# Performance work log

Hardware: AMD Instinct MI355X
Metric: run time of the kernel (lower is better)

The kernel has to match this reference:

```python
import jax, jax.numpy as jnp
import numpy as np


def setup_inputs() -> dict:
    key = jax.random.key(0)
    k1, k2 = jax.random.split(key)
    N, D, K = 262144, 64, 1024
    residual = jax.random.normal(k1, (N, D), dtype=jnp.float32)
    # nn.init.uniform_(codebook.weight, -1/K, 1/K)
    codebook = jax.random.uniform(k2, (K, D), dtype=jnp.float32,
                                  minval=-1.0 / K, maxval=1.0 / K)
    return {"residual": residual, "codebook": codebook}


def reference(residual, codebook):
    # squared L2 distances via ||a||^2 + ||b||^2 - 2 a.b (argmin-equivalent to
    # the broadcast (N,K,D) form, without materializing it)
    r2 = jnp.sum(residual * residual, axis=1, keepdims=True)        # (N, 1)
    c2 = jnp.sum(codebook * codebook, axis=1)[None, :]              # (1, K)
    dists = r2 + c2 - 2.0 * (residual @ codebook.T)                 # (N, K)
    codes = jnp.argmin(dists, axis=1)                               # (N,) int
    quantized = codebook[codes]                                     # (N, D)
    return quantized, codes
```

## Files before the change

kernel.cpp:

```cpp
#include <hip/hip_runtime.h>
#include <float.h>

#define D 64

typedef float f32x4 __attribute__((ext_vector_type(4)));
typedef _Float16 f16x8 __attribute__((ext_vector_type(8)));

__device__ __forceinline__ float np_sum_sq_64(const float* v) {
  float s[8];
#pragma unroll
  for (int j = 0; j < 8; ++j) s[j] = __fmul_rn(v[j], v[j]);
#pragma unroll
  for (int b = 1; b < 8; ++b) {
#pragma unroll
    for (int j = 0; j < 8; ++j)
      s[j] = __fadd_rn(s[j], __fmul_rn(v[8 * b + j], v[8 * b + j]));
  }
  float t01 = __fadd_rn(s[0], s[1]);
  float t23 = __fadd_rn(s[2], s[3]);
  float t45 = __fadd_rn(s[4], s[5]);
  float t67 = __fadd_rn(s[6], s[7]);
  return __fadd_rn(__fadd_rn(t01, t23), __fadd_rn(t45, t67));
}

__device__ __forceinline__ unsigned int pkh(float a, float b) {
  union { _Float16 h[2]; unsigned int u; } x;
  x.h[0] = (_Float16)a;
  x.h[1] = (_Float16)b;
  return x.u;
}

__global__ __launch_bounds__(64) void vq_prep(
    const float* __restrict__ cb, unsigned short* __restrict__ cbh,
    float4* __restrict__ cbT4, float* __restrict__ c2,
    float* __restrict__ c2n, unsigned int* __restrict__ counters, int K) {
  if (blockIdx.x == 0 && threadIdx.x == 0) { counters[0] = 0u; counters[1] = 0u; }
  int k = blockIdx.x * 64 + threadIdx.x;
  if (k >= K) return;
  float row[D];
  const float4* cp = (const float4*)(cb + (size_t)k * D);
#pragma unroll
  for (int i = 0; i < 16; ++i) {
    float4 v = cp[i];
    row[4 * i] = v.x; row[4 * i + 1] = v.y;
    row[4 * i + 2] = v.z; row[4 * i + 3] = v.w;
    cbT4[(size_t)i * K + k] = v;
    *(uint2*)(cbh + (size_t)k * D + 4 * i) =
        make_uint2(pkh(v.x * 1024.f, v.y * 1024.f),
                   pkh(v.z * 1024.f, v.w * 1024.f));
  }
  float c2v = np_sum_sq_64(row);
  c2[k] = c2v;
  c2n[k] = -512.0f * c2v;
}

__global__ __launch_bounds__(256, 3) void vq_screen(
    const float* __restrict__ residual, const float* __restrict__ codebook,
    const unsigned short* __restrict__ cbh, const float* __restrict__ c2n,
    const float* __restrict__ c2, float* __restrict__ out_q,
    float* __restrict__ codes_f, unsigned int* __restrict__ counters,
    int* __restrict__ list, int N, int K) {
  __shared__ unsigned short smem[4096];
  __shared__ float red[768];
  __shared__ int code_lds[64];
  __shared__ float srow[64];

  int tid = threadIdx.x;
  int rowbase = blockIdx.x * 64;

  float sr4[4];
#pragma unroll
  for (int jj = 0; jj < 4; ++jj) {
    int i = tid + 256 * jj;
    int r = i >> 4, d0 = (i & 15) * 4;
    float4 v = *(const float4*)(residual + (size_t)(rowbase + r) * D + d0);
    sr4[jj] = fabsf(v.x) + fabsf(v.y) + fabsf(v.z) + fabsf(v.w);
    int tile = r >> 4, rr = r & 15;
    int kblk = d0 >> 5, kk = d0 & 31;
    int lanep = rr + 16 * (kk >> 3);
    int off = ((tile * 2 + kblk) * 64 + lanep) * 8 + (kk & 7);
    *(uint2*)(smem + off) = make_uint2(pkh(v.x, v.y), pkh(v.z, v.w));
  }
#pragma unroll
  for (int jj = 0; jj < 4; ++jj) {
    float s = sr4[jj];
    s += __shfl_xor(s, 1, 64);
    s += __shfl_xor(s, 2, 64);
    s += __shfl_xor(s, 4, 64);
    s += __shfl_xor(s, 8, 64);
    sr4[jj] = s;
  }
  if ((tid & 15) == 0) {
#pragma unroll
    for (int jj = 0; jj < 4; ++jj) srow[(tid >> 4) + 16 * jj] = sr4[jj];
  }
  __syncthreads();

  int w = tid >> 6, lane = tid & 63;
  int lane15 = lane & 15, lq = lane >> 4;

  f16x8 ah[4][2];
#pragma unroll
  for (int t = 0; t < 4; ++t)
#pragma unroll
    for (int kb = 0; kb < 2; ++kb)
      ah[t][kb] = *(const f16x8*)(smem + ((t * 2 + kb) * 64 + lane) * 8);

  float m1[4][4], m2[4][4], m3[4][4];
#pragma unroll
  for (int t = 0; t < 4; ++t)
#pragma unroll
    for (int j = 0; j < 4; ++j) {
      m1[t][j] = -FLT_MAX; m2[t][j] = -FLT_MAX; m3[t][j] = -FLT_MAX;
    }

  const unsigned short* ph = cbh + (size_t)(w * 16 + lane15) * D + lq * 8;
  const float* pc2 = c2n + (w * 16 + lane15);

  f16x8 B0a = *(const f16x8*)(ph);
  f16x8 B1a = *(const f16x8*)(ph + 32);
  float c2a = *pc2;
  ph += 64 * D; pc2 += 64;
  f16x8 B0b = *(const f16x8*)(ph);
  f16x8 B1b = *(const f16x8*)(ph + 32);
  float c2b = *pc2;

  unsigned int idb = (unsigned int)((w << 4) | lane15);
  for (int cc = 0; cc < 16; ++cc) {
    f16x8 ch0 = B0a, ch1 = B1a;
    float q = c2a;
    B0a = B0b; B1a = B1b; c2a = c2b;
    if (cc < 14) {
      ph += 64 * D; pc2 += 64;
      B0b = *(const f16x8*)(ph);
      B1b = *(const f16x8*)(ph + 32);
      c2b = *pc2;
    }

#pragma unroll
    for (int t = 0; t < 4; ++t) {
      f32x4 a = {q, q, q, q};
      a = __builtin_amdgcn_mfma_f32_16x16x32_f16(ah[t][0], ch0, a, 0, 0, 0);
      a = __builtin_amdgcn_mfma_f32_16x16x32_f16(ah[t][1], ch1, a, 0, 0, 0);
#pragma unroll
      for (int j = 0; j < 4; ++j) {
        float spf = __uint_as_float((__float_as_uint(a[j]) & 0xFFFFFC00u) | idb);
        float o1 = m1[t][j], o2 = m2[t][j];
        m3[t][j] = __builtin_amdgcn_fmed3f(o2, m3[t][j], spf);
        m2[t][j] = __builtin_amdgcn_fmed3f(o1, o2, spf);
        m1[t][j] = fmaxf(o1, spf);
      }
    }
    idb += 64u;
  }

#pragma unroll
  for (int dlt = 1; dlt < 16; dlt <<= 1) {
#pragma unroll
    for (int t = 0; t < 4; ++t)
#pragma unroll
      for (int j = 0; j < 4; ++j) {
        float a1 = m1[t][j], a2 = m2[t][j], a3 = m3[t][j];
        float b1 = __shfl_xor(a1, dlt, 64);
        float b2 = __shfl_xor(a2, dlt, 64);
        float b3 = __shfl_xor(a3, dlt, 64);
        m1[t][j] = fmaxf(a1, b1);
        m2[t][j] = fmaxf(fminf(a1, b1), fmaxf(a2, b2));
        m3[t][j] = fmaxf(fmaxf(fminf(a2, b1), fminf(a1, b2)), fmaxf(a3, b3));
      }
  }

  if (lane15 == 0) {
#pragma unroll
    for (int t = 0; t < 4; ++t)
#pragma unroll
      for (int j = 0; j < 4; ++j) {
        int r = t * 16 + lq * 4 + j;
        int base = (w * 64 + r) * 3;
        red[base + 0] = m1[t][j];
        red[base + 1] = m2[t][j];
        red[base + 2] = m3[t][j];
      }
  }
  __syncthreads();
  if (tid < 64) {
    float a1 = red[tid * 3 + 0], a2 = red[tid * 3 + 1], a3 = red[tid * 3 + 2];
#pragma unroll
    for (int wv = 1; wv < 4; ++wv) {
      float b1 = red[(wv * 64 + tid) * 3 + 0];
      float b2 = red[(wv * 64 + tid) * 3 + 1];
      float b3 = red[(wv * 64 + tid) * 3 + 2];
      float n1 = fmaxf(a1, b1);
      float n2 = fmaxf(fminf(a1, b1), fmaxf(a2, b2));
      float n3 = fmaxf(fmaxf(fminf(a2, b1), fminf(a1, b2)), fmaxf(a3, b3));
      a1 = n1; a2 = n2; a3 = n3;
    }
    unsigned int u1 = __float_as_uint(a1);
    unsigned int u2 = __float_as_uint(a2);
    unsigned int u3 = __float_as_uint(a3);
    int ka = (int)(u1 & 1023u);
    float g1 = __uint_as_float(u1 & 0xFFFFFC00u);
    float g2 = __uint_as_float(u2 & 0xFFFFFC00u);
    float g3 = __uint_as_float(u3 & 0xFFFFFC00u);
    float margin = __builtin_fmaf(srow[tid], 2.3552e-3f, 2.048e-2f);
    int row = rowbase + tid;
    int win = ka;
    if (g1 - g2 < margin) {
      if (g1 - g3 < margin) {
        unsigned int s = atomicAdd(counters + 0, 1u);
        list[s] = row;
      } else {
        int kb = (int)(u2 & 1023u);
        float r[D];
        const float4* rp = (const float4*)(residual + ((size_t)row << 6));
#pragma unroll
        for (int qq = 0; qq < 16; ++qq) {
          float4 v = rp[qq];
          r[4 * qq] = v.x; r[4 * qq + 1] = v.y;
          r[4 * qq + 2] = v.z; r[4 * qq + 3] = v.w;
        }
        float r2 = np_sum_sq_64(r);
        float da = 0.f, db = 0.f;
        const float4* ap = (const float4*)(codebook + ((size_t)ka << 6));
        const float4* bp = (const float4*)(codebook + ((size_t)kb << 6));
#pragma unroll
        for (int qq = 0; qq < 16; ++qq) {
          float4 x = ap[qq], y = bp[qq];
          da = __fmaf_rn(r[4 * qq + 0], x.x, da); db = __fmaf_rn(r[4 * qq + 0], y.x, db);
          da = __fmaf_rn(r[4 * qq + 1], x.y, da); db = __fmaf_rn(r[4 * qq + 1], y.y, db);
          da = __fmaf_rn(r[4 * qq + 2], x.z, da); db = __fmaf_rn(r[4 * qq + 2], y.z, db);
          da = __fmaf_rn(r[4 * qq + 3], x.w, da); db = __fmaf_rn(r[4 * qq + 3], y.w, db);
        }
        float dista = __fsub_rn(__fadd_rn(r2, c2[ka]), __fmul_rn(2.0f, da));
        float distb = __fsub_rn(__fadd_rn(r2, c2[kb]), __fmul_rn(2.0f, db));
        bool bwin = (distb < dista) || (distb == dista && kb < ka);
        win = bwin ? kb : ka;
      }
    }
    code_lds[tid] = win;
    codes_f[row] = (float)win;
  }
  __syncthreads();

  for (int e = tid; e < 4096; e += 256) {
    int r = e >> 6, d = e & 63;
    out_q[(size_t)rowbase * D + e] = codebook[((size_t)code_lds[r] << 6) + d];
  }
}

__global__ __launch_bounds__(256) void vq_rescore(
    const float* __restrict__ residual, const float* __restrict__ codebook,
    const float4* __restrict__ cbT4, const float* __restrict__ c2,
    float* __restrict__ codes_f, float* __restrict__ out_q,
    const unsigned int* __restrict__ counters,
    const int* __restrict__ list, int K) {
  unsigned int cnt = counters[0];
  int w = threadIdx.x >> 6, lane = threadIdx.x & 63;
  unsigned int npairs = (cnt + 1) >> 1;
  for (unsigned int g = blockIdx.x * 4 + w; g < npairs; g += gridDim.x * 4) {
    int n0 = list[2 * g];
    bool two = (2 * g + 1 < cnt);
    int n1 = two ? list[2 * g + 1] : n0;

    float rl0 = residual[(size_t)n0 * D + lane];
    float rl1 = residual[(size_t)n1 * D + lane];

    int j = lane & 7;
    float x0 = __shfl(rl0, j, 64), x1 = __shfl(rl1, j, 64);
    float s0 = __fmul_rn(x0, x0), s1 = __fmul_rn(x1, x1);
#pragma unroll
    for (int b = 1; b < 8; ++b) {
      x0 = __shfl(rl0, 8 * b + j, 64);
      x1 = __shfl(rl1, 8 * b + j, 64);
      s0 = __fadd_rn(s0, __fmul_rn(x0, x0));
      s1 = __fadd_rn(s1, __fmul_rn(x1, x1));
    }
    s0 = __fadd_rn(s0, __shfl_xor(s0, 1, 64));
    s1 = __fadd_rn(s1, __shfl_xor(s1, 1, 64));
    s0 = __fadd_rn(s0, __shfl_xor(s0, 2, 64));
    s1 = __fadd_rn(s1, __shfl_xor(s1, 2, 64));
    s0 = __fadd_rn(s0, __shfl_xor(s0, 4, 64));
    s1 = __fadd_rn(s1, __shfl_xor(s1, 4, 64));
    float r2_0 = s0, r2_1 = s1;

    float m0[16], m1v[16];
#pragma unroll
    for (int ch = 0; ch < 16; ++ch) { m0[ch] = 0.f; m1v[ch] = 0.f; }

    for (int d4 = 0; d4 < 16; ++d4) {
      float a0 = __shfl(rl0, 4 * d4, 64), b0 = __shfl(rl0, 4 * d4 + 1, 64);
      float c0 = __shfl(rl0, 4 * d4 + 2, 64), e0 = __shfl(rl0, 4 * d4 + 3, 64);
      float a1 = __shfl(rl1, 4 * d4, 64), b1 = __shfl(rl1, 4 * d4 + 1, 64);
      float c1 = __shfl(rl1, 4 * d4 + 2, 64), e1 = __shfl(rl1, 4 * d4 + 3, 64);
      const float4* bp = cbT4 + (size_t)d4 * K + lane;
      float4 cbv[8];
#pragma unroll
      for (int h = 0; h < 2; ++h) {
#pragma unroll
        for (int q = 0; q < 8; ++q) cbv[q] = bp[(h * 8 + q) * 64];
#pragma unroll
        for (int q = 0; q < 8; ++q) {
          int ch = h * 8 + q;
          float4 c = cbv[q];
          float t0 = m0[ch], t1 = m1v[ch];
          t0 = __fmaf_rn(a0, c.x, t0); t1 = __fmaf_rn(a1, c.x, t1);
          t0 = __fmaf_rn(b0, c.y, t0); t1 = __fmaf_rn(b1, c.y, t1);
          t0 = __fmaf_rn(c0, c.z, t0); t1 = __fmaf_rn(c1, c.z, t1);
          t0 = __fmaf_rn(e0, c.w, t0); t1 = __fmaf_rn(e1, c.w, t1);
          m0[ch] = t0; m1v[ch] = t1;
        }
      }
    }

    float best0 = FLT_MAX, best1 = FLT_MAX;
    int bk0 = 0, bk1 = 0;
#pragma unroll
    for (int ch = 0; ch < 16; ++ch) {
      int code = ch * 64 + lane;
      float c2v = c2[code];
      float d0 = __fsub_rn(__fadd_rn(r2_0, c2v), __fmul_rn(2.0f, m0[ch]));
      float d1 = __fsub_rn(__fadd_rn(r2_1, c2v), __fmul_rn(2.0f, m1v[ch]));
      if (d0 < best0) { best0 = d0; bk0 = code; }
      if (d1 < best1) { best1 = d1; bk1 = code; }
    }
#pragma unroll
    for (int off = 32; off > 0; off >>= 1) {
      float ob = __shfl_down(best0, off, 64);
      int oi = __shfl_down(bk0, off, 64);
      if (ob < best0 || (ob == best0 && oi < bk0)) { best0 = ob; bk0 = oi; }
      ob = __shfl_down(best1, off, 64);
      oi = __shfl_down(bk1, off, 64);
      if (ob < best1 || (ob == best1 && oi < bk1)) { best1 = ob; bk1 = oi; }
    }
    int k0 = __shfl(bk0, 0, 64);
    int k1 = __shfl(bk1, 0, 64);
    if (lane == 0) codes_f[n0] = (float)k0;
    out_q[(size_t)n0 * D + lane] = codebook[((size_t)k0 << 6) + lane];
    if (two) {
      if (lane == 0) codes_f[n1] = (float)k1;
      out_q[(size_t)n1 * D + lane] = codebook[((size_t)k1 << 6) + lane];
    }
  }
}

extern "C" void kernel_launch(void* const* d_in, const int* in_sizes, int n_in,
                              void* d_out, int out_size, void* d_ws, size_t ws_size,
                              hipStream_t stream) {
  const float* residual = (const float*)d_in[0];
  const float* codebook = (const float*)d_in[1];
  int N = in_sizes[0] / D;
  int K = in_sizes[1] / D;

  float* out_q = (float*)d_out;
  float* codes_f = out_q + (size_t)N * D;

  char* ws = (char*)d_ws;
  float* c2 = (float*)ws;
  float* c2n = (float*)(ws + (size_t)K * 4);
  unsigned short* cbh = (unsigned short*)(ws + (size_t)K * 8);
  float4* cbT4 = (float4*)(ws + (size_t)K * 8 + (size_t)K * D * 2);
  unsigned int* counters =
      (unsigned int*)(ws + (size_t)K * 8 + (size_t)K * D * 2 + (size_t)K * D * 4);
  int* list = (int*)(counters + 2);

  vq_prep<<<(K + 63) / 64, 64, 0, stream>>>(codebook, cbh, cbT4, c2, c2n,
                                            counters, K);

  vq_screen<<<N / 64, 256, 0, stream>>>(residual, codebook, cbh, c2n, c2,
                                        out_q, codes_f, counters, list, N, K);

  vq_rescore<<<512, 256, 0, stream>>>(residual, codebook, cbT4, c2, codes_f,
                                      out_q, counters, list, K);
}
```

Measured before the change: 225.4 us.

## Fuse full rescoring of ambiguous rows into the screening kernel

Ambiguous rows whose top-three fp16 scores fall within the margin are no longer appended to a global list for a separate rescore kernel. They are queued in shared memory and rescored exactly by the block's own wavefronts before the final gather. This removes a kernel launch, the global atomic counter and list, and the second write of out_q for those rows. In exchange, blocks with many ambiguous rows stall their whole block, the screen kernel's register pressure may rise, and each wave now rescores one row at a time instead of two.

```diff
diff --git a/kernel.cpp b/kernel.cpp
--- a/kernel.cpp
+++ b/kernel.cpp
@@ -33,8 +33,7 @@
 __global__ __launch_bounds__(64) void vq_prep(
     const float* __restrict__ cb, unsigned short* __restrict__ cbh,
     float4* __restrict__ cbT4, float* __restrict__ c2,
-    float* __restrict__ c2n, unsigned int* __restrict__ counters, int K) {
-  if (blockIdx.x == 0 && threadIdx.x == 0) { counters[0] = 0u; counters[1] = 0u; }
+    float* __restrict__ c2n, int K) {
   int k = blockIdx.x * 64 + threadIdx.x;
   if (k >= K) return;
   float row[D];
@@ -57,16 +56,18 @@
 __global__ __launch_bounds__(256, 3) void vq_screen(
     const float* __restrict__ residual, const float* __restrict__ codebook,
     const unsigned short* __restrict__ cbh, const float* __restrict__ c2n,
-    const float* __restrict__ c2, float* __restrict__ out_q,
-    float* __restrict__ codes_f, unsigned int* __restrict__ counters,
-    int* __restrict__ list, int N, int K) {
+    const float* __restrict__ c2, const float4* __restrict__ cbT4,
+    float* __restrict__ out_q, float* __restrict__ codes_f, int N, int K) {
   __shared__ unsigned short smem[4096];
   __shared__ float red[768];
   __shared__ int code_lds[64];
   __shared__ float srow[64];
+  __shared__ int qrows[64];
+  __shared__ int qcnt;
 
   int tid = threadIdx.x;
   int rowbase = blockIdx.x * 64;
+  if (tid == 0) qcnt = 0;
 
   float sr4[4];
 #pragma unroll
@@ -205,10 +206,12 @@
     float margin = __builtin_fmaf(srow[tid], 2.3552e-3f, 2.048e-2f);
     int row = rowbase + tid;
     int win = ka;
+    bool clustered = false;
     if (g1 - g2 < margin) {
       if (g1 - g3 < margin) {
-        unsigned int s = atomicAdd(counters + 0, 1u);
-        list[s] = row;
+        clustered = true;
+        int s = atomicAdd(&qcnt, 1);
+        qrows[s] = tid;
       } else {
         int kb = (int)(u2 & 1023u);
         float r[D];
@@ -237,61 +240,40 @@
         win = bwin ? kb : ka;
       }
     }
-    code_lds[tid] = win;
-    codes_f[row] = (float)win;
+    if (!clustered) {
+      code_lds[tid] = win;
+      codes_f[row] = (float)win;
+    }
   }
   __syncthreads();
 
-  for (int e = tid; e < 4096; e += 256) {
-    int r = e >> 6, d = e & 63;
-    out_q[(size_t)rowbase * D + e] = codebook[((size_t)code_lds[r] << 6) + d];
-  }
-}
-
-__global__ __launch_bounds__(256) void vq_rescore(
-    const float* __restrict__ residual, const float* __restrict__ codebook,
-    const float4* __restrict__ cbT4, const float* __restrict__ c2,
-    float* __restrict__ codes_f, float* __restrict__ out_q,
-    const unsigned int* __restrict__ counters,
-    const int* __restrict__ list, int K) {
-  unsigned int cnt = counters[0];
-  int w = threadIdx.x >> 6, lane = threadIdx.x & 63;
-  unsigned int npairs = (cnt + 1) >> 1;
-  for (unsigned int g = blockIdx.x * 4 + w; g < npairs; g += gridDim.x * 4) {
-    int n0 = list[2 * g];
-    bool two = (2 * g + 1 < cnt);
-    int n1 = two ? list[2 * g + 1] : n0;
-
-    float rl0 = residual[(size_t)n0 * D + lane];
-    float rl1 = residual[(size_t)n1 * D + lane];
+  int nq = qcnt;
+  for (int base = 0; base < nq; base += 4) {
+    int myi = base + w;
+    bool act = (myi < nq);
+    int rloc = qrows[act ? myi : 0];
+    float rl0 = residual[(size_t)(rowbase + rloc) * D + lane];
 
     int j = lane & 7;
-    float x0 = __shfl(rl0, j, 64), x1 = __shfl(rl1, j, 64);
-    float s0 = __fmul_rn(x0, x0), s1 = __fmul_rn(x1, x1);
+    float x0 = __shfl(rl0, j, 64);
+    float s0 = __fmul_rn(x0, x0);
 #pragma unroll
     for (int b = 1; b < 8; ++b) {
       x0 = __shfl(rl0, 8 * b + j, 64);
-      x1 = __shfl(rl1, 8 * b + j, 64);
       s0 = __fadd_rn(s0, __fmul_rn(x0, x0));
-      s1 = __fadd_rn(s1, __fmul_rn(x1, x1));
     }
     s0 = __fadd_rn(s0, __shfl_xor(s0, 1, 64));
-    s1 = __fadd_rn(s1, __shfl_xor(s1, 1, 64));
     s0 = __fadd_rn(s0, __shfl_xor(s0, 2, 64));
-    s1 = __fadd_rn(s1, __shfl_xor(s1, 2, 64));
     s0 = __fadd_rn(s0, __shfl_xor(s0, 4, 64));
-    s1 = __fadd_rn(s1, __shfl_xor(s1, 4, 64));
-    float r2_0 = s0, r2_1 = s1;
-
-    float m0[16], m1v[16];
-#pragma unroll
-    for (int ch = 0; ch < 16; ++ch) { m0[ch] = 0.f; m1v[ch] = 0.f; }
+    float r2_0 = s0;
+
+    float m0[16];
+#pragma unroll
+    for (int ch = 0; ch < 16; ++ch) m0[ch] = 0.f;
 
     for (int d4 = 0; d4 < 16; ++d4) {
       float a0 = __shfl(rl0, 4 * d4, 64), b0 = __shfl(rl0, 4 * d4 + 1, 64);
       float c0 = __shfl(rl0, 4 * d4 + 2, 64), e0 = __shfl(rl0, 4 * d4 + 3, 64);
-      float a1 = __shfl(rl1, 4 * d4, 64), b1 = __shfl(rl1, 4 * d4 + 1, 64);
-      float c1 = __shfl(rl1, 4 * d4 + 2, 64), e1 = __shfl(rl1, 4 * d4 + 3, 64);
       const float4* bp = cbT4 + (size_t)d4 * K + lane;
       float4 cbv[8];
 #pragma unroll
@@ -302,44 +284,42 @@
         for (int q = 0; q < 8; ++q) {
           int ch = h * 8 + q;
           float4 c = cbv[q];
-          float t0 = m0[ch], t1 = m1v[ch];
-          t0 = __fmaf_rn(a0, c.x, t0); t1 = __fmaf_rn(a1, c.x, t1);
-          t0 = __fmaf_rn(b0, c.y, t0); t1 = __fmaf_rn(b1, c.y, t1);
-          t0 = __fmaf_rn(c0, c.z, t0); t1 = __fmaf_rn(c1, c.z, t1);
-          t0 = __fmaf_rn(e0, c.w, t0); t1 = __fmaf_rn(e1, c.w, t1);
-          m0[ch] = t0; m1v[ch] = t1;
+          float t0 = m0[ch];
+          t0 = __fmaf_rn(a0, c.x, t0);
+          t0 = __fmaf_rn(b0, c.y, t0);
+          t0 = __fmaf_rn(c0, c.z, t0);
+          t0 = __fmaf_rn(e0, c.w, t0);
+          m0[ch] = t0;
         }
       }
     }
 
-    float best0 = FLT_MAX, best1 = FLT_MAX;
-    int bk0 = 0, bk1 = 0;
+    float best0 = FLT_MAX;
+    int bk0 = 0;
 #pragma unroll
     for (int ch = 0; ch < 16; ++ch) {
       int code = ch * 64 + lane;
       float c2v = c2[code];
       float d0 = __fsub_rn(__fadd_rn(r2_0, c2v), __fmul_rn(2.0f, m0[ch]));
-      float d1 = __fsub_rn(__fadd_rn(r2_1, c2v), __fmul_rn(2.0f, m1v[ch]));
       if (d0 < best0) { best0 = d0; bk0 = code; }
-      if (d1 < best1) { best1 = d1; bk1 = code; }
     }
 #pragma unroll
     for (int off = 32; off > 0; off >>= 1) {
       float ob = __shfl_down(best0, off, 64);
       int oi = __shfl_down(bk0, off, 64);
       if (ob < best0 || (ob == best0 && oi < bk0)) { best0 = ob; bk0 = oi; }
-      ob = __shfl_down(best1, off, 64);
-      oi = __shfl_down(bk1, off, 64);
-      if (ob < best1 || (ob == best1 && oi < bk1)) { best1 = ob; bk1 = oi; }
     }
     int k0 = __shfl(bk0, 0, 64);
-    int k1 = __shfl(bk1, 0, 64);
-    if (lane == 0) codes_f[n0] = (float)k0;
-    out_q[(size_t)n0 * D + lane] = codebook[((size_t)k0 << 6) + lane];
-    if (two) {
-      if (lane == 0) codes_f[n1] = (float)k1;
-      out_q[(size_t)n1 * D + lane] = codebook[((size_t)k1 << 6) + lane];
-    }
+    if (act) {
+      code_lds[rloc] = k0;
+      if (lane == 0) codes_f[rowbase + rloc] = (float)k0;
+    }
+  }
+  __syncthreads();
+
+  for (int e = tid; e < 4096; e += 256) {
+    int r = e >> 6, d = e & 63;
+    out_q[(size_t)rowbase * D + e] = codebook[((size_t)code_lds[r] << 6) + d];
   }
 }
 
@@ -359,16 +339,9 @@
   float* c2n = (float*)(ws + (size_t)K * 4);
   unsigned short* cbh = (unsigned short*)(ws + (size_t)K * 8);
   float4* cbT4 = (float4*)(ws + (size_t)K * 8 + (size_t)K * D * 2);
-  unsigned int* counters =
-      (unsigned int*)(ws + (size_t)K * 8 + (size_t)K * D * 2 + (size_t)K * D * 4);
-  int* list = (int*)(counters + 2);
-
-  vq_prep<<<(K + 63) / 64, 64, 0, stream>>>(codebook, cbh, cbT4, c2, c2n,
-                                            counters, K);
+
+  vq_prep<<<(K + 63) / 64, 64, 0, stream>>>(codebook, cbh, cbT4, c2, c2n, K);
 
   vq_screen<<<N / 64, 256, 0, stream>>>(residual, codebook, cbh, c2n, c2,
-                                        out_q, codes_f, counters, list, N, K);
-
-  vq_rescore<<<512, 256, 0, stream>>>(residual, codebook, cbT4, c2, codes_f,
-                                      out_q, counters, list, K);
-}
+                                        cbT4, out_q, codes_f, N, K);
+}
```

Measured after the change: 263.9 us. +17.1%, slower.
